# Optimization experiments

Hardware: AMD Instinct MI355X
Metric: run time of the kernel (lower is better)

## Reference

```python
import jax, jax.numpy as jnp
import numpy as np

L = 4          # num_layers
D = 512        # d_model
NH = 8         # num_heads
DH = 64        # d_head
DFF = 2048     # d_ff
EPS = 1e-5     # nn.LayerNorm default eps


def _layer_norm(x, g, b):
    m = x.mean(axis=-1, keepdims=True)
    v = ((x - m) ** 2).mean(axis=-1, keepdims=True)
    return (x - m) / jnp.sqrt(v + EPS) * g + b


def setup_inputs() -> dict:
    key = jax.random.key(0)
    ks = jax.random.split(key, 14)
    s = 0.02
    z = jax.random.normal(ks[0], (4, 16, D, 8, 8), dtype=jnp.float32)
    Wq = s * jax.random.normal(ks[1], (L, D, NH * DH), dtype=jnp.float32)
    Wk = s * jax.random.normal(ks[2], (L, D, NH * DH), dtype=jnp.float32)
    Wv = s * jax.random.normal(ks[3], (L, D, NH * DH), dtype=jnp.float32)
    Wo = s * jax.random.normal(ks[4], (L, NH * DH, D), dtype=jnp.float32)
    W1 = s * jax.random.normal(ks[5], (L, D, DFF), dtype=jnp.float32)
    b1 = jnp.zeros((L, DFF), dtype=jnp.float32)
    W2 = s * jax.random.normal(ks[6], (L, DFF, D), dtype=jnp.float32)
    b2 = jnp.zeros((L, D), dtype=jnp.float32)
    ln1_g = jnp.ones((L, D), dtype=jnp.float32)
    ln1_b = jnp.zeros((L, D), dtype=jnp.float32)
    ln2_g = jnp.ones((L, D), dtype=jnp.float32)
    ln2_b = jnp.zeros((L, D), dtype=jnp.float32)
    return {"z": z, "Wq": Wq, "Wk": Wk, "Wv": Wv, "Wo": Wo,
            "W1": W1, "b1": b1, "W2": W2, "b2": b2,
            "ln1_g": ln1_g, "ln1_b": ln1_b, "ln2_g": ln2_g, "ln2_b": ln2_b}


def _forward(z, Wq, Wk, Wv, Wo, W1, b1, W2, b2, ln1_g, ln1_b, ln2_g, ln2_b):
    B, T, Dm, H, W = z.shape
    N = H * W
    Tp = T * N  # T' = t*h*w
    # sinusoidal positional embedding over T' positions
    pos = jnp.arange(Tp, dtype=z.dtype)
    inv_freq = 1.0 / (10000.0 ** (jnp.arange(0, Dm, 2, dtype=z.dtype) / Dm))
    si = pos[:, None] * inv_freq[None, :]                 # (T', D/2)
    pos_emb = jnp.concatenate([jnp.sin(si), jnp.cos(si)], axis=-1)[:, None, :]  # (T',1,D)
    # rearrange 'b t d h w -> (t h w) b d'
    x = jnp.transpose(z, (1, 3, 4, 0, 2)).reshape(Tp, B, Dm)
    x = x + pos_emb
    # block-causal mask at block size N (True = masked)
    blk = jnp.arange(Tp) // N
    mask = blk[None, :] > blk[:, None]                    # (T'_q, T'_k)
    scale = 1.0 / np.sqrt(DH)
    outs = []
    for l in range(L):
        # post-lnorm multi-head attention (LN applied before residual add)
        q = (x @ Wq[l]).reshape(Tp, B, NH, DH)
        k = (x @ Wk[l]).reshape(Tp, B, NH, DH)
        v = (x @ Wv[l]).reshape(Tp, B, NH, DH)
        s = jnp.einsum('ibnd,jbnd->ijbn', q, k) * scale
        s = jnp.where(mask[:, :, None, None], -jnp.inf, s)
        p = jax.nn.softmax(s, axis=1)
        av = jnp.einsum('ijbn,jbnd->ibnd', p, v).reshape(Tp, B, NH * DH)
        attn = _layer_norm(av @ Wo[l], ln1_g[l], ln1_b[l])
        x = attn + x
        ff = _layer_norm(jax.nn.relu(x @ W1[l] + b1[l]) @ W2[l] + b2[l], ln2_g[l], ln2_b[l])
        x = ff + x
        outs.append(x)
    out = jnp.stack(outs, axis=1)                         # (T', L, B, D)
    # rearrange '(t h w) l b d -> b t l d h w'
    out = out.reshape(T, H, W, L, B, Dm)
    return jnp.transpose(out, (4, 0, 3, 5, 1, 2))


def reference(z, Wq, Wk, Wv, Wo, W1, b1, W2, b2, ln1_g, ln1_b, ln2_g, ln2_b):
    return _forward(z, Wq, Wk, Wv, Wo, W1, b1, W2, b2, ln1_g, ln1_b, ln2_g, ln2_b)
```

## Files before the change

kernel.cpp:

```cpp
#include <hip/hip_runtime.h>
#include <hip/hip_bf16.h>
#include <math.h>


#define TP 1024
#define BB 4
#define DD 512
#define DHEAD 64
#define DFF 2048
#define MROWS (TP*BB)
#define EPS 1e-5f
#define CSC 0.18033688011112042f

typedef __attribute__((ext_vector_type(8))) short bf16x8;
typedef __attribute__((ext_vector_type(4))) float f32x4;

__device__ __forceinline__ float b2f(unsigned short u) {
    union { unsigned int i; float f; } z; z.i = ((unsigned int)u) << 16; return z.f;
}
__device__ __forceinline__ unsigned short f2bu(float f) {
    __hip_bfloat16 h = __float2bfloat16(f);
    return *reinterpret_cast<unsigned short*>(&h);
}

#define WAITV0() asm volatile("s_waitcnt vmcnt(0)" ::: "memory")
#define WAITV4() asm volatile("s_waitcnt vmcnt(4)" ::: "memory")
#define WAITV8() asm volatile("s_waitcnt vmcnt(8)" ::: "memory")
#define WAITL0() asm volatile("s_waitcnt lgkmcnt(0)" ::: "memory")
__device__ __forceinline__ void hard_barrier() {
    __builtin_amdgcn_sched_barrier(0);
    __builtin_amdgcn_s_barrier();
    __builtin_amdgcn_sched_barrier(0);
}
#define GLOAD(gp, lp) __builtin_amdgcn_global_load_lds( \
    (const __attribute__((address_space(1))) void*)(gp), \
    (__attribute__((address_space(3))) void*)(lp), 16, 0, 0)

__device__ __forceinline__ int fsw(int row) { return (row ^ (row >> 2)) & 3; }

__global__ __launch_bounds__(256) void embed_kernel(const float* __restrict__ z,
                                                    float* __restrict__ x,
                                                    __hip_bfloat16* __restrict__ x_bf) {
    __shared__ float tile[64][65];
    const int blk = blockIdx.x;
    const int dc = blk & 7, b = (blk >> 3) & 3, t = blk >> 5;
    const int tid = threadIdx.x;
#pragma unroll
    for (int it = 0; it < 4; ++it) {
        int idx = it * 256 + tid;
        int d_i = idx >> 4, hw4 = (idx & 15) * 4;
        int d = dc * 64 + d_i;
        float4 v = *reinterpret_cast<const float4*>(
            z + ((size_t)((b * 16 + t) * 512 + d)) * 64 + hw4);
        int j = d & 255;
        float freq = expf(-(float)(2 * j) * (9.210340371976184f / 512.0f));
        int i0 = t * 64 + hw4;
#pragma unroll
        for (int e = 0; e < 4; ++e) {
            float si = (float)(i0 + e) * freq;
            float pe = (d < 256) ? sinf(si) : cosf(si);
            tile[d_i][hw4 + e] = ((&v.x)[e]) + pe;
        }
    }
    __syncthreads();
#pragma unroll
    for (int it = 0; it < 4; ++it) {
        int idx = it * 256 + tid;
        int hw_o = idx >> 4, dq = (idx & 15) * 4;
        int row = (t * 64 + hw_o) * 4 + b;
        float4 v = make_float4(tile[dq][hw_o], tile[dq + 1][hw_o],
                               tile[dq + 2][hw_o], tile[dq + 3][hw_o]);
        *reinterpret_cast<float4*>(x + (size_t)row * 512 + dc * 64 + dq) = v;
        ushort4 u;
        u.x = f2bu(v.x); u.y = f2bu(v.y); u.z = f2bu(v.z); u.w = f2bu(v.w);
        *reinterpret_cast<ushort4*>((unsigned short*)x_bf + (size_t)row * 512 + dc * 64 + dq) = u;
    }
}

__global__ __launch_bounds__(256) void wt_convert(
    const float* __restrict__ Wq, const float* __restrict__ Wk,
    const float* __restrict__ Wv, const float* __restrict__ Wo,
    const float* __restrict__ W1, const float* __restrict__ W2,
    __hip_bfloat16* __restrict__ wall) {
    __shared__ float tile[32][33];
    const int l = blockIdx.y;
    __hip_bfloat16* wl = wall + (size_t)l * (4 * 512 * 512 + 2 * 512 * 2048);
    int b = blockIdx.x;
    const float* src; __hip_bfloat16* dst; int R, C, local, cbs;
    if (b < 1024) {
        int m = b >> 8; local = b & 255; R = 512; C = 512; cbs = 4;
        src = ((m == 0) ? Wq : (m == 1) ? Wk : (m == 2) ? Wv : Wo) + (size_t)l * 512 * 512;
        dst = wl + m * 512 * 512;
    } else if (b < 2048) {
        local = b - 1024; R = 512; C = 2048; cbs = 6;
        src = W1 + (size_t)l * 512 * 2048; dst = wl + 4 * 512 * 512;
    } else {
        local = b - 2048; R = 2048; C = 512; cbs = 4;
        src = W2 + (size_t)l * 2048 * 512; dst = wl + 4 * 512 * 512 + 512 * 2048;
    }
    int bx = local & ((1 << cbs) - 1), by = local >> cbs;
    int tx = threadIdx.x & 31, ty = threadIdx.x >> 5;
#pragma unroll
    for (int j = 0; j < 4; ++j)
        tile[ty + j * 8][tx] = src[(size_t)(by * 32 + ty + j * 8) * C + bx * 32 + tx];
    __syncthreads();
#pragma unroll
    for (int j = 0; j < 4; ++j)
        dst[(size_t)(bx * 32 + ty + j * 8) * R + by * 32 + tx] =
            __float2bfloat16(tile[tx][ty + j * 8]);
}

template<bool BIAS, bool RELU, bool OUT_BF16>
__global__ __launch_bounds__(256) void gemm_k(const __hip_bfloat16* __restrict__ A,
                                              const __hip_bfloat16* __restrict__ Bt,
                                              const float* __restrict__ bias,
                                              void* __restrict__ Cout,
                                              int N, int K, int ntx) {
    __shared__ __hip_bfloat16 As[2][128 * 32];
    __shared__ __hip_bfloat16 Bs[2][128 * 32];

    const int lb = blockIdx.x;
    const int wg = (lb & 7) * (gridDim.x >> 3) + (lb >> 3);
    const int m0 = (wg / ntx) * 128;
    const int n0 = (wg % ntx) * 128;

    const int tid  = threadIdx.x;
    const int wave = tid >> 6;
    const int lane = tid & 63;
    const int lr   = lane & 15;
    const int hi   = lane >> 4;
    const int lk   = (hi ^ fsw(lr)) << 3;
    const int wr   = (wave >> 1) * 64;
    const int wc   = (wave & 1) * 64;

    f32x4 acc[4][4];
#pragma unroll
    for (int i = 0; i < 4; ++i)
#pragma unroll
        for (int j = 0; j < 4; ++j) acc[i][j] = (f32x4){0.f, 0.f, 0.f, 0.f};

    const int c0 = tid, c1 = tid + 256;
    const __hip_bfloat16* a0 = A  + (size_t)(m0 + (c0 >> 2)) * K + (((c0 & 3) ^ fsw(c0 >> 2)) << 3);
    const __hip_bfloat16* a1 = A  + (size_t)(m0 + (c1 >> 2)) * K + (((c1 & 3) ^ fsw(c1 >> 2)) << 3);
    const __hip_bfloat16* b0 = Bt + (size_t)(n0 + (c0 >> 2)) * K + (((c0 & 3) ^ fsw(c0 >> 2)) << 3);
    const __hip_bfloat16* b1 = Bt + (size_t)(n0 + (c1 >> 2)) * K + (((c1 & 3) ^ fsw(c1 >> 2)) << 3);
    const int o0 = wave * 512, o1 = 2048 + wave * 512;

    GLOAD(a0, &As[0][o0]); GLOAD(a1, &As[0][o1]);
    GLOAD(b0, &Bs[0][o0]); GLOAD(b1, &Bs[0][o1]);
    WAITV0();
    hard_barrier();

    for (int k0 = 0; k0 < K; k0 += 32) {
        const int buf = (k0 >> 5) & 1;
        if (k0 + 32 < K) {
            GLOAD(a0 + k0 + 32, &As[buf ^ 1][o0]); GLOAD(a1 + k0 + 32, &As[buf ^ 1][o1]);
            GLOAD(b0 + k0 + 32, &Bs[buf ^ 1][o0]); GLOAD(b1 + k0 + 32, &Bs[buf ^ 1][o1]);
        }
        bf16x8 af[4], bfv[4];
#pragma unroll
        for (int i = 0; i < 4; ++i)
            af[i] = *reinterpret_cast<const bf16x8*>(&As[buf][(size_t)(wr + i * 16 + lr) * 32 + lk]);
#pragma unroll
        for (int j = 0; j < 4; ++j)
            bfv[j] = *reinterpret_cast<const bf16x8*>(&Bs[buf][(size_t)(wc + j * 16 + lr) * 32 + lk]);
#pragma unroll
        for (int i = 0; i < 4; ++i)
#pragma unroll
            for (int j = 0; j < 4; ++j)
                acc[i][j] = __builtin_amdgcn_mfma_f32_16x16x32_bf16(af[i], bfv[j], acc[i][j], 0, 0, 0);
        WAITV0();
        hard_barrier();
    }

#pragma unroll
    for (int j = 0; j < 4; ++j) {
        int col = n0 + wc + j * 16 + lr;
        float bv = BIAS ? bias[col] : 0.0f;
#pragma unroll
        for (int i = 0; i < 4; ++i) {
            int row = m0 + wr + i * 16 + (hi << 2);
#pragma unroll
            for (int r = 0; r < 4; ++r) {
                float v = acc[i][j][r] + bv;
                if (RELU) v = fmaxf(v, 0.0f);
                if (OUT_BF16)
                    ((unsigned short*)Cout)[(size_t)(row + r) * N + col] = f2bu(v);
                else
                    ((float*)Cout)[(size_t)(row + r) * N + col] = v;
            }
        }
    }
}

template<bool BIAS, bool RELU, bool OUT_BF16>
__device__ __forceinline__ void gemm64_body(const __hip_bfloat16* __restrict__ A,
                                            const __hip_bfloat16* __restrict__ Bt,
                                            const float* __restrict__ bias,
                                            void* __restrict__ Cout, int K,
                                            float scale,
                                            __hip_bfloat16* As, __hip_bfloat16* Bs) {
    const int lb = blockIdx.x;
    const int wg = (lb & 7) * (gridDim.x >> 3) + (lb >> 3);
    const int m0 = (wg >> 3) * 64;
    const int n0 = (wg & 7) * 64;

    const int tid  = threadIdx.x;
    const int wave = tid >> 6;
    const int lane = tid & 63;
    const int lr   = lane & 15;
    const int hi   = lane >> 4;
    const int lk   = (hi ^ fsw(lr)) << 3;
    const int wr   = (wave >> 1) * 32;
    const int wc   = (wave & 1) * 32;

    f32x4 acc[2][2];
#pragma unroll
    for (int i = 0; i < 2; ++i)
#pragma unroll
        for (int j = 0; j < 2; ++j) acc[i][j] = (f32x4){0.f, 0.f, 0.f, 0.f};

    const __hip_bfloat16* ag = A  + (size_t)(m0 + (tid >> 2)) * K + (((tid & 3) ^ fsw(tid >> 2)) << 3);
    const __hip_bfloat16* bg = Bt + (size_t)(n0 + (tid >> 2)) * K + (((tid & 3) ^ fsw(tid >> 2)) << 3);
    const int wo = wave * 512;

    GLOAD(ag, As + wo); GLOAD(bg, Bs + wo);
    WAITV0();
    hard_barrier();

    for (int k0 = 0; k0 < K; k0 += 32) {
        const int buf = (k0 >> 5) & 1;
        if (k0 + 32 < K) {
            GLOAD(ag + k0 + 32, As + (buf ^ 1) * 2048 + wo);
            GLOAD(bg + k0 + 32, Bs + (buf ^ 1) * 2048 + wo);
        }
        const __hip_bfloat16* Ab = As + buf * 2048;
        const __hip_bfloat16* Bb = Bs + buf * 2048;
        bf16x8 af[2], bfv[2];
#pragma unroll
        for (int i = 0; i < 2; ++i)
            af[i] = *reinterpret_cast<const bf16x8*>(&Ab[(size_t)(wr + i * 16 + lr) * 32 + lk]);
#pragma unroll
        for (int j = 0; j < 2; ++j)
            bfv[j] = *reinterpret_cast<const bf16x8*>(&Bb[(size_t)(wc + j * 16 + lr) * 32 + lk]);
#pragma unroll
        for (int i = 0; i < 2; ++i)
#pragma unroll
            for (int j = 0; j < 2; ++j)
                acc[i][j] = __builtin_amdgcn_mfma_f32_16x16x32_bf16(af[i], bfv[j], acc[i][j], 0, 0, 0);
        WAITV0();
        hard_barrier();
    }

#pragma unroll
    for (int j = 0; j < 2; ++j) {
        int col = n0 + wc + j * 16 + lr;
        float bv = BIAS ? bias[col] : 0.0f;
#pragma unroll
        for (int i = 0; i < 2; ++i) {
            int row = m0 + wr + i * 16 + (hi << 2);
#pragma unroll
            for (int r = 0; r < 4; ++r) {
                float v = acc[i][j][r] * scale + bv;
                if (RELU) v = fmaxf(v, 0.0f);
                if (OUT_BF16)
                    ((unsigned short*)Cout)[(size_t)(row + r) * 512 + col] = f2bu(v);
                else
                    ((float*)Cout)[(size_t)(row + r) * 512 + col] = v;
            }
        }
    }
}

template<bool BIAS, bool RELU, bool OUT_BF16>
__global__ __launch_bounds__(256) void gemm64_k(const __hip_bfloat16* __restrict__ A,
                                                const __hip_bfloat16* __restrict__ Bt,
                                                const float* __restrict__ bias,
                                                void* __restrict__ Cout, int K) {
    __shared__ __hip_bfloat16 As[2 * 64 * 32];
    __shared__ __hip_bfloat16 Bs[2 * 64 * 32];
    gemm64_body<BIAS, RELU, OUT_BF16>(A, Bt, bias, Cout, K, 1.0f, As, Bs);
}

__global__ __launch_bounds__(256) void gemm_qkv64(const __hip_bfloat16* __restrict__ A,
                                                  const __hip_bfloat16* __restrict__ B0,
                                                  const __hip_bfloat16* __restrict__ B1,
                                                  const __hip_bfloat16* __restrict__ B2,
                                                  __hip_bfloat16* __restrict__ C0,
                                                  __hip_bfloat16* __restrict__ C1,
                                                  __hip_bfloat16* __restrict__ C2) {
    __shared__ __hip_bfloat16 As[2 * 64 * 32];
    __shared__ __hip_bfloat16 Bs[2 * 64 * 32];
    int sel = blockIdx.z;
    const __hip_bfloat16* Bt = (sel == 0) ? B0 : (sel == 1) ? B1 : B2;
    __hip_bfloat16* C = (sel == 0) ? C0 : (sel == 1) ? C1 : C2;
    float scale = (sel == 0) ? CSC : 1.0f;
    gemm64_body<false, false, true>(A, Bt, nullptr, (void*)C, 512, scale, As, Bs);
}

__global__ __launch_bounds__(256) void transpose_v(const unsigned short* __restrict__ v,
                                                   unsigned short* __restrict__ vt) {
    __shared__ unsigned short t[64][72];
    const int kb = blockIdx.x;
    const int bn = blockIdx.y;
    const int b = bn >> 3, n = bn & 7;
    const int tid = threadIdx.x;
#pragma unroll
    for (int it = 0; it < 2; ++it) {
        int c = tid + it * 256;
        int row = c >> 3, d0 = (c & 7) * 8;
        const unsigned short* src =
            v + ((size_t)((kb * 64 + row) * 4 + b)) * 512 + n * 64 + d0;
        bf16x8 xv = *reinterpret_cast<const bf16x8*>(src);
#pragma unroll
        for (int e = 0; e < 8; ++e) t[row][d0 + e] = (unsigned short)xv[e];
    }
    __syncthreads();
#pragma unroll
    for (int it = 0; it < 2; ++it) {
        int c = tid + it * 256;
        int d = c >> 3, k0 = (c & 7) * 8;
        bf16x8 o;
#pragma unroll
        for (int e = 0; e < 8; ++e) o[e] = (short)t[k0 + e][d];
        *reinterpret_cast<bf16x8*>(vt + ((size_t)(bn * 64 + d)) * 1024 + kb * 64 + k0) = o;
    }
}

__device__ __forceinline__ int aswz(int row, int col) {
    return (row * 64 + col) ^ ((row & 7) << 3);
}

__device__ __forceinline__ void stage_tile(const unsigned short* gbase, int stride,
                                           unsigned short* lds, int wave, int tid) {
#pragma unroll
    for (int it = 0; it < 2; ++it) {
        int c = tid + it * 256;
        int row = c >> 3;
        int i = (c & 7) ^ (row & 7);
        const unsigned short* g = gbase + (size_t)row * stride + i * 8;
        __builtin_amdgcn_global_load_lds(
            (const __attribute__((address_space(1))) void*)g,
            (__attribute__((address_space(3))) void*)(lds + it * 2048 + wave * 512),
            16, 0, 0);
    }
}

__global__ __launch_bounds__(256) void attn_mfma(const unsigned short* __restrict__ q,
                                                 const unsigned short* __restrict__ k,
                                                 const unsigned short* __restrict__ vt,
                                                 unsigned short* __restrict__ av) {
    __shared__ unsigned short Qs[64 * 64];
    __shared__ unsigned short Ks[4][64 * 64];
    __shared__ unsigned short Vts[4][64 * 64];
    __shared__ unsigned short Ps[64 * 64];

    const int tid = threadIdx.x;
    const int wave = tid >> 6, lane = tid & 63;
    const int lr = lane & 15, hi = lane >> 4;
    const int wr = wave * 16;

    const int p = blockIdx.x;
    const int xcd = p & 7, idx = p >> 3;
    const int bn = xcd * 4 + (idx & 3);
    const int qb = 15 - (idx >> 2);
    const int b = bn >> 3, n = bn & 7;

    const unsigned short* kcol  = k  + (size_t)b * 512 + n * 64;
    const unsigned short* vtrow = vt + (size_t)(bn * 64) * 1024;

    stage_tile(q + ((size_t)(qb * 64) * 4 + b) * 512 + n * 64, 2048, Qs, wave, tid);
    stage_tile(kcol, 2048, Ks[0], wave, tid);
    stage_tile(vtrow, 1024, Vts[0], wave, tid);
    if (qb >= 1) {
        stage_tile(kcol + (size_t)64 * 2048, 2048, Ks[1], wave, tid);
        stage_tile(vtrow + 64, 1024, Vts[1], wave, tid);
    }
    if (qb >= 2) {
        stage_tile(kcol + (size_t)128 * 2048, 2048, Ks[2], wave, tid);
        stage_tile(vtrow + 128, 1024, Vts[2], wave, tid);
    }

    f32x4 o_acc[4], l_acc;
#pragma unroll
    for (int db = 0; db < 4; ++db) o_acc[db] = (f32x4){0.f, 0.f, 0.f, 0.f};
    l_acc = (f32x4){0.f, 0.f, 0.f, 0.f};

    bf16x8 onesf;
#pragma unroll
    for (int e = 0; e < 8; ++e) onesf[e] = (short)0x3F80;

    bf16x8 qf[2];

    for (int kb = 0; kb <= qb; ++kb) {
        const int ahead = (qb - kb >= 2) ? 2 : (qb - kb);
        if (ahead == 2) WAITV8();
        else if (ahead == 1) WAITV4();
        else WAITV0();
        hard_barrier();
        if (kb + 3 <= qb) {
            stage_tile(kcol + (size_t)(kb + 3) * 64 * 2048, 2048,
                       Ks[(kb + 3) & 3], wave, tid);
            stage_tile(vtrow + (kb + 3) * 64, 1024, Vts[(kb + 3) & 3], wave, tid);
        }
        if (kb == 0) {
#pragma unroll
            for (int ks = 0; ks < 2; ++ks)
                qf[ks] = *reinterpret_cast<const bf16x8*>(
                    (const unsigned short*)Qs + aswz(wr + lr, ks * 32 + hi * 8));
        }
        const unsigned short* Kb = Ks[kb & 3];
        const unsigned short* Vb = Vts[kb & 3];

        f32x4 sf[4];
#pragma unroll
        for (int jb = 0; jb < 4; ++jb) sf[jb] = (f32x4){0.f, 0.f, 0.f, 0.f};
        __builtin_amdgcn_s_setprio(1);
#pragma unroll
        for (int ks = 0; ks < 2; ++ks) {
            bf16x8 a = qf[ks];
#pragma unroll
            for (int jb = 0; jb < 4; ++jb) {
                bf16x8 kf = *reinterpret_cast<const bf16x8*>(
                    Kb + aswz(jb * 16 + lr, ks * 32 + hi * 8));
                sf[jb] = __builtin_amdgcn_mfma_f32_16x16x32_bf16(a, kf, sf[jb], 0, 0, 0);
            }
        }
        __builtin_amdgcn_s_setprio(0);

#pragma unroll
        for (int jb = 0; jb < 4; ++jb)
#pragma unroll
            for (int r = 0; r < 4; ++r) {
                float pe = exp2f(fminf(sf[jb][r], 100.0f));
                Ps[aswz(wr + 4 * hi + r, jb * 16 + lr)] = f2bu(pe);
            }
        WAITL0();
        hard_barrier();

        __builtin_amdgcn_s_setprio(1);
#pragma unroll
        for (int ks = 0; ks < 2; ++ks) {
            bf16x8 pf = *reinterpret_cast<const bf16x8*>(
                (const unsigned short*)Ps + aswz(wr + lr, ks * 32 + hi * 8));
            l_acc = __builtin_amdgcn_mfma_f32_16x16x32_bf16(pf, onesf, l_acc, 0, 0, 0);
#pragma unroll
            for (int db = 0; db < 4; ++db) {
                bf16x8 vf = *reinterpret_cast<const bf16x8*>(
                    Vb + aswz(db * 16 + lr, ks * 32 + hi * 8));
                o_acc[db] = __builtin_amdgcn_mfma_f32_16x16x32_bf16(pf, vf, o_acc[db], 0, 0, 0);
            }
        }
        __builtin_amdgcn_s_setprio(0);
    }

#pragma unroll
    for (int r = 0; r < 4; ++r) {
        float inv = 1.0f / l_acc[r];
        int row = qb * 64 + wr + 4 * hi + r;
#pragma unroll
        for (int db = 0; db < 4; ++db)
            av[((size_t)row * 4 + b) * 512 + n * 64 + db * 16 + lr] =
                f2bu(o_acc[db][r] * inv);
    }
}

__global__ __launch_bounds__(64) void add_ln_kernel(const float* __restrict__ y,
                                                    const float* __restrict__ g,
                                                    const float* __restrict__ bta,
                                                    float* __restrict__ x,
                                                    __hip_bfloat16* __restrict__ x_bf) {
    const int row = blockIdx.x;
    const int tid = threadIdx.x;
    const float* yr = y + (size_t)row * DD;
    float4 v0 = *reinterpret_cast<const float4*>(&yr[tid * 4]);
    float4 v1 = *reinterpret_cast<const float4*>(&yr[256 + tid * 4]);
    float s = v0.x + v0.y + v0.z + v0.w + v1.x + v1.y + v1.z + v1.w;
    float ss = v0.x * v0.x + v0.y * v0.y + v0.z * v0.z + v0.w * v0.w +
               v1.x * v1.x + v1.y * v1.y + v1.z * v1.z + v1.w * v1.w;
#pragma unroll
    for (int off = 32; off; off >>= 1) {
        s  += __shfl_xor(s, off);
        ss += __shfl_xor(ss, off);
    }
    float mean = s * (1.0f / 512.0f);
    float var = ss * (1.0f / 512.0f) - mean * mean;
    float rstd = rsqrtf(var + EPS);

    float* xr = x + (size_t)row * DD;
    float vals[8] = {v0.x, v0.y, v0.z, v0.w, v1.x, v1.y, v1.z, v1.w};
#pragma unroll
    for (int e = 0; e < 8; ++e) {
        int d = (e < 4) ? (tid * 4 + e) : (256 + tid * 4 + (e - 4));
        float nrm = (vals[e] - mean) * rstd * g[d] + bta[d];
        float xo = xr[d] + nrm;
        xr[d] = xo;
        x_bf[(size_t)row * DD + d] = __float2bfloat16(xo);
    }
}

__global__ __launch_bounds__(256) void out_transpose(const float* __restrict__ x,
                                                     float* __restrict__ out, int l) {
    __shared__ float tile[64][65];
    const int blk = blockIdx.x;
    const int dc = blk & 7;
    const int b  = (blk >> 3) & 3;
    const int t  = blk >> 5;
    const int tid = threadIdx.x;
#pragma unroll
    for (int it = 0; it < 4; ++it) {
        int c = tid + it * 256;
        int hw = c >> 4, f4 = c & 15;
        const float* src = x + (size_t)((t * 64 + hw) * 4 + b) * 512 + dc * 64 + f4 * 4;
        float4 v = *reinterpret_cast<const float4*>(src);
        tile[hw][f4 * 4 + 0] = v.x; tile[hw][f4 * 4 + 1] = v.y;
        tile[hw][f4 * 4 + 2] = v.z; tile[hw][f4 * 4 + 3] = v.w;
    }
    __syncthreads();
    size_t ob = (((size_t)(b * 16 + t) * 4 + l) * 512 + dc * 64) * 64;
#pragma unroll
    for (int it = 0; it < 4; ++it) {
        int c = tid + it * 256;
        int d = c >> 4, f4 = c & 15;
        float4 v = make_float4(tile[f4 * 4 + 0][d], tile[f4 * 4 + 1][d],
                               tile[f4 * 4 + 2][d], tile[f4 * 4 + 3][d]);
        *reinterpret_cast<float4*>(out + ob + (size_t)d * 64 + f4 * 4) = v;
    }
}

extern "C" void kernel_launch(void* const* d_in, const int* in_sizes, int n_in,
                              void* d_out, int out_size, void* d_ws, size_t ws_size,
                              hipStream_t stream) {
    const float* z    = (const float*)d_in[0];
    const float* Wq   = (const float*)d_in[1];
    const float* Wk   = (const float*)d_in[2];
    const float* Wv   = (const float*)d_in[3];
    const float* Wo   = (const float*)d_in[4];
    const float* W1   = (const float*)d_in[5];
    const float* b1   = (const float*)d_in[6];
    const float* W2   = (const float*)d_in[7];
    const float* b2   = (const float*)d_in[8];
    const float* ln1g = (const float*)d_in[9];
    const float* ln1b = (const float*)d_in[10];
    const float* ln2g = (const float*)d_in[11];
    const float* ln2b = (const float*)d_in[12];
    float* out = (float*)d_out;

    const size_t MB = 1u << 20;
    char* base = (char*)d_ws;
    float*          x     = (float*)(base);
    __hip_bfloat16* x_bf  = (__hip_bfloat16*)(base + 8  * MB);
    __hip_bfloat16* q_bf  = (__hip_bfloat16*)(base + 12 * MB);
    __hip_bfloat16* k_bf  = (__hip_bfloat16*)(base + 16 * MB);
    __hip_bfloat16* v_bf  = (__hip_bfloat16*)(base + 20 * MB);
    __hip_bfloat16* av_bf = (__hip_bfloat16*)(base + 24 * MB);
    float*          tmp   = (float*)(base + 28 * MB);
    __hip_bfloat16* wall  = (__hip_bfloat16*)(base + 36 * MB);
    __hip_bfloat16* ff1_bf = q_bf;
    unsigned short* vt    = (unsigned short*)tmp;

    const size_t WL = 4 * 512 * 512 + 2 * 512 * 2048;

    embed_kernel<<<512, 256, 0, stream>>>(z, x, x_bf);
    wt_convert<<<dim3(3072, 4), 256, 0, stream>>>(Wq, Wk, Wv, Wo, W1, W2, wall);

    for (int l = 0; l < 4; ++l) {
        __hip_bfloat16* wl  = wall + (size_t)l * WL;
        __hip_bfloat16* wqt = wl;
        __hip_bfloat16* wkt = wqt + 512 * 512;
        __hip_bfloat16* wvt = wkt + 512 * 512;
        __hip_bfloat16* wot = wvt + 512 * 512;
        __hip_bfloat16* w1t = wot + 512 * 512;
        __hip_bfloat16* w2t = w1t + 512 * 2048;

        gemm_qkv64<<<dim3(512, 1, 3), 256, 0, stream>>>(x_bf, wqt, wkt, wvt,
                                                        q_bf, k_bf, v_bf);

        transpose_v<<<dim3(16, 32), 256, 0, stream>>>((const unsigned short*)v_bf, vt);

        attn_mfma<<<512, 256, 0, stream>>>(
            (const unsigned short*)q_bf, (const unsigned short*)k_bf,
            vt, (unsigned short*)av_bf);

        gemm64_k<false, false, false><<<512, 256, 0, stream>>>(
            av_bf, wot, nullptr, (void*)tmp, 512);
        add_ln_kernel<<<MROWS, 64, 0, stream>>>(tmp, ln1g + l * 512, ln1b + l * 512,
                                                x, x_bf);

        gemm_k<true, true, true><<<512, 256, 0, stream>>>(
            x_bf, w1t, b1 + l * 2048, (void*)ff1_bf, 2048, 512, 16);
        gemm64_k<true, false, false><<<512, 256, 0, stream>>>(
            ff1_bf, w2t, b2 + l * 512, (void*)tmp, 2048);
        add_ln_kernel<<<MROWS, 64, 0, stream>>>(tmp, ln2g + l * 512, ln2b + l * 512,
                                                x, x_bf);
        out_transpose<<<512, 256, 0, stream>>>(x, out, l);
    }
}
```

Measured before the change: 465.2 us.

## Deepen GEMM pipelines to 4-stage LDS ring with wider K tiles and setprio

Both GEMM kernels move from a double-buffered LDS pipeline to a 4-buffer ring with three stages in flight. The wait uses partial vmcnt counts so the barrier no longer drains every outstanding load each iteration. The 64x64 GEMM also doubles its K step to 64 with a new XOR swizzle, and both kernels raise wave priority around the MFMA block. The aim is to hide global-load latency and cut barrier and wait overhead, in exchange for more LDS per block (64KB for the 128 GEMM), which may lower occupancy.

New measurement: 439.8 us. -5.5%, faster.

```diff
diff --git a/kernel.cpp b/kernel.cpp
--- a/kernel.cpp
+++ b/kernel.cpp
@@ -31,6 +31,11 @@
     __builtin_amdgcn_sched_barrier(0);
     __builtin_amdgcn_s_barrier();
     __builtin_amdgcn_sched_barrier(0);
+}
+__device__ __forceinline__ void waitv_ahead(int ahead) {
+    if (ahead == 2) WAITV8();
+    else if (ahead == 1) WAITV4();
+    else WAITV0();
 }
 #define GLOAD(gp, lp) __builtin_amdgcn_global_load_lds( \
     (const __attribute__((address_space(1))) void*)(gp), \
@@ -116,8 +121,8 @@
                                               const float* __restrict__ bias,
                                               void* __restrict__ Cout,
                                               int N, int K, int ntx) {
-    __shared__ __hip_bfloat16 As[2][128 * 32];
-    __shared__ __hip_bfloat16 Bs[2][128 * 32];
+    __shared__ __hip_bfloat16 As[4][128 * 32];
+    __shared__ __hip_bfloat16 Bs[4][128 * 32];
 
     const int lb = blockIdx.x;
     const int wg = (lb & 7) * (gridDim.x >> 3) + (lb >> 3);
@@ -146,17 +151,23 @@
     const __hip_bfloat16* b1 = Bt + (size_t)(n0 + (c1 >> 2)) * K + (((c1 & 3) ^ fsw(c1 >> 2)) << 3);
     const int o0 = wave * 512, o1 = 2048 + wave * 512;
 
-    GLOAD(a0, &As[0][o0]); GLOAD(a1, &As[0][o1]);
-    GLOAD(b0, &Bs[0][o0]); GLOAD(b1, &Bs[0][o1]);
-    WAITV0();
-    hard_barrier();
-
-    for (int k0 = 0; k0 < K; k0 += 32) {
-        const int buf = (k0 >> 5) & 1;
-        if (k0 + 32 < K) {
-            GLOAD(a0 + k0 + 32, &As[buf ^ 1][o0]); GLOAD(a1 + k0 + 32, &As[buf ^ 1][o1]);
-            GLOAD(b0 + k0 + 32, &Bs[buf ^ 1][o0]); GLOAD(b1 + k0 + 32, &Bs[buf ^ 1][o1]);
-        }
+    const int nst = K >> 5;
+#pragma unroll
+    for (int s = 0; s < 3; ++s) {
+        GLOAD(a0 + s * 32, &As[s][o0]); GLOAD(a1 + s * 32, &As[s][o1]);
+        GLOAD(b0 + s * 32, &Bs[s][o0]); GLOAD(b1 + s * 32, &Bs[s][o1]);
+    }
+
+    for (int k = 0; k < nst; ++k) {
+        const int ahead = (nst - 1 - k >= 2) ? 2 : (nst - 1 - k);
+        waitv_ahead(ahead);
+        hard_barrier();
+        if (k + 3 < nst) {
+            const int kk = (k + 3) << 5, bb = (k + 3) & 3;
+            GLOAD(a0 + kk, &As[bb][o0]); GLOAD(a1 + kk, &As[bb][o1]);
+            GLOAD(b0 + kk, &Bs[bb][o0]); GLOAD(b1 + kk, &Bs[bb][o1]);
+        }
+        const int buf = k & 3;
         bf16x8 af[4], bfv[4];
 #pragma unroll
         for (int i = 0; i < 4; ++i)
@@ -164,13 +175,13 @@
 #pragma unroll
         for (int j = 0; j < 4; ++j)
             bfv[j] = *reinterpret_cast<const bf16x8*>(&Bs[buf][(size_t)(wc + j * 16 + lr) * 32 + lk]);
+        __builtin_amdgcn_s_setprio(1);
 #pragma unroll
         for (int i = 0; i < 4; ++i)
 #pragma unroll
             for (int j = 0; j < 4; ++j)
                 acc[i][j] = __builtin_amdgcn_mfma_f32_16x16x32_bf16(af[i], bfv[j], acc[i][j], 0, 0, 0);
-        WAITV0();
-        hard_barrier();
+        __builtin_amdgcn_s_setprio(0);
     }
 
 #pragma unroll
@@ -210,7 +221,6 @@
     const int lane = tid & 63;
     const int lr   = lane & 15;
     const int hi   = lane >> 4;
-    const int lk   = (hi ^ fsw(lr)) << 3;
     const int wr   = (wave >> 1) * 32;
     const int wc   = (wave & 1) * 32;
 
@@ -220,36 +230,57 @@
 #pragma unroll
         for (int j = 0; j < 2; ++j) acc[i][j] = (f32x4){0.f, 0.f, 0.f, 0.f};
 
-    const __hip_bfloat16* ag = A  + (size_t)(m0 + (tid >> 2)) * K + (((tid & 3) ^ fsw(tid >> 2)) << 3);
-    const __hip_bfloat16* bg = Bt + (size_t)(n0 + (tid >> 2)) * K + (((tid & 3) ^ fsw(tid >> 2)) << 3);
-    const int wo = wave * 512;
-
-    GLOAD(ag, As + wo); GLOAD(bg, Bs + wo);
-    WAITV0();
-    hard_barrier();
-
-    for (int k0 = 0; k0 < K; k0 += 32) {
-        const int buf = (k0 >> 5) & 1;
-        if (k0 + 32 < K) {
-            GLOAD(ag + k0 + 32, As + (buf ^ 1) * 2048 + wo);
-            GLOAD(bg + k0 + 32, Bs + (buf ^ 1) * 2048 + wo);
-        }
-        const __hip_bfloat16* Ab = As + buf * 2048;
-        const __hip_bfloat16* Bb = Bs + buf * 2048;
-        bf16x8 af[2], bfv[2];
-#pragma unroll
-        for (int i = 0; i < 2; ++i)
-            af[i] = *reinterpret_cast<const bf16x8*>(&Ab[(size_t)(wr + i * 16 + lr) * 32 + lk]);
-#pragma unroll
-        for (int j = 0; j < 2; ++j)
-            bfv[j] = *reinterpret_cast<const bf16x8*>(&Bb[(size_t)(wc + j * 16 + lr) * 32 + lk]);
-#pragma unroll
-        for (int i = 0; i < 2; ++i)
-#pragma unroll
-            for (int j = 0; j < 2; ++j)
-                acc[i][j] = __builtin_amdgcn_mfma_f32_16x16x32_bf16(af[i], bfv[j], acc[i][j], 0, 0, 0);
-        WAITV0();
+    const int c0 = tid, c1 = tid + 256;
+    const __hip_bfloat16* a0 = A  + (size_t)(m0 + (c0 >> 3)) * K + (((c0 & 7) ^ ((c0 >> 3) & 7)) << 3);
+    const __hip_bfloat16* a1 = A  + (size_t)(m0 + (c1 >> 3)) * K + (((c1 & 7) ^ ((c1 >> 3) & 7)) << 3);
+    const __hip_bfloat16* b0 = Bt + (size_t)(n0 + (c0 >> 3)) * K + (((c0 & 7) ^ ((c0 >> 3) & 7)) << 3);
+    const __hip_bfloat16* b1 = Bt + (size_t)(n0 + (c1 >> 3)) * K + (((c1 & 7) ^ ((c1 >> 3) & 7)) << 3);
+    const int o0 = wave * 512, o1 = 2048 + wave * 512;
+
+    const int nst = K >> 6;
+#pragma unroll
+    for (int s = 0; s < 3; ++s) {
+        if (s < 3 && s < nst) {
+            GLOAD(a0 + s * 64, As + s * 4096 + o0); GLOAD(a1 + s * 64, As + s * 4096 + o1);
+            GLOAD(b0 + s * 64, Bs + s * 4096 + o0); GLOAD(b1 + s * 64, Bs + s * 4096 + o1);
+        }
+    }
+
+    for (int k = 0; k < nst; ++k) {
+        const int ahead = (nst - 1 - k >= 2) ? 2 : (nst - 1 - k);
+        waitv_ahead(ahead);
         hard_barrier();
+        if (k + 3 < nst) {
+            const int kk = (k + 3) << 6;
+            const int bo = ((k + 3) & 3) * 4096;
+            GLOAD(a0 + kk, As + bo + o0); GLOAD(a1 + kk, As + bo + o1);
+            GLOAD(b0 + kk, Bs + bo + o0); GLOAD(b1 + kk, Bs + bo + o1);
+        }
+        const __hip_bfloat16* Ab = As + (k & 3) * 4096;
+        const __hip_bfloat16* Bb = Bs + (k & 3) * 4096;
+        __builtin_amdgcn_s_setprio(1);
+#pragma unroll
+        for (int ks = 0; ks < 2; ++ks) {
+            bf16x8 af[2], bfv[2];
+#pragma unroll
+            for (int i = 0; i < 2; ++i) {
+                int row = wr + i * 16 + lr;
+                af[i] = *reinterpret_cast<const bf16x8*>(
+                    &Ab[(size_t)row * 64 + (((ks * 4 + hi) ^ (row & 7)) << 3)]);
+            }
+#pragma unroll
+            for (int j = 0; j < 2; ++j) {
+                int row = wc + j * 16 + lr;
+                bfv[j] = *reinterpret_cast<const bf16x8*>(
+                    &Bb[(size_t)row * 64 + (((ks * 4 + hi) ^ (row & 7)) << 3)]);
+            }
+#pragma unroll
+            for (int i = 0; i < 2; ++i)
+#pragma unroll
+                for (int j = 0; j < 2; ++j)
+                    acc[i][j] = __builtin_amdgcn_mfma_f32_16x16x32_bf16(af[i], bfv[j], acc[i][j], 0, 0, 0);
+        }
+        __builtin_amdgcn_s_setprio(0);
     }
 
 #pragma unroll
@@ -277,8 +308,8 @@
                                                 const __hip_bfloat16* __restrict__ Bt,
                                                 const float* __restrict__ bias,
                                                 void* __restrict__ Cout, int K) {
-    __shared__ __hip_bfloat16 As[2 * 64 * 32];
-    __shared__ __hip_bfloat16 Bs[2 * 64 * 32];
+    __shared__ __hip_bfloat16 As[4 * 64 * 64];
+    __shared__ __hip_bfloat16 Bs[4 * 64 * 64];
     gemm64_body<BIAS, RELU, OUT_BF16>(A, Bt, bias, Cout, K, 1.0f, As, Bs);
 }
 
@@ -289,8 +320,8 @@
                                                   __hip_bfloat16* __restrict__ C0,
                                                   __hip_bfloat16* __restrict__ C1,
                                                   __hip_bfloat16* __restrict__ C2) {
-    __shared__ __hip_bfloat16 As[2 * 64 * 32];
-    __shared__ __hip_bfloat16 Bs[2 * 64 * 32];
+    __shared__ __hip_bfloat16 As[4 * 64 * 64];
+    __shared__ __hip_bfloat16 Bs[4 * 64 * 64];
     int sel = blockIdx.z;
     const __hip_bfloat16* Bt = (sel == 0) ? B0 : (sel == 1) ? B1 : B2;
     __hip_bfloat16* C = (sel == 0) ? C0 : (sel == 1) ? C1 : C2;
@@ -394,9 +425,7 @@
 
     for (int kb = 0; kb <= qb; ++kb) {
         const int ahead = (qb - kb >= 2) ? 2 : (qb - kb);
-        if (ahead == 2) WAITV8();
-        else if (ahead == 1) WAITV4();
-        else WAITV0();
+        waitv_ahead(ahead);
         hard_barrier();
         if (kb + 3 <= qb) {
             stage_tile(kcol + (size_t)(kb + 3) * 64 * 2048, 2048,
```
